# Kernel tuning notes

Hardware: AMD Instinct MI355X
Metric: run time of the kernel (lower is better)

The kernel has to match this reference:

```python
import jax, jax.numpy as jnp
import numpy as np

MODEL_DIM = 512
HEAD_NUM = 8
HEAD_DIM = 64
INNER_DIM = HEAD_NUM * HEAD_DIM  # 512
B, L, S = 4, 2048, 2048


def setup_inputs() -> dict:
    key = jax.random.key(0)
    ks = jax.random.split(key, 7)
    query = jax.random.normal(ks[0], (B, L, MODEL_DIM), dtype=jnp.float32)
    key_t = jax.random.normal(ks[1], (B, S, MODEL_DIM), dtype=jnp.float32)
    value = jax.random.normal(ks[2], (B, S, MODEL_DIM), dtype=jnp.float32)
    # nn.Linear weights stored as [out, in]; applied as x @ W.T
    sc = 1.0 / np.sqrt(MODEL_DIM)
    Wq = jax.random.uniform(ks[3], (INNER_DIM, MODEL_DIM), jnp.float32, -sc, sc)
    Wk = jax.random.uniform(ks[4], (INNER_DIM, MODEL_DIM), jnp.float32, -sc, sc)
    Wv = jax.random.uniform(ks[5], (INNER_DIM, MODEL_DIM), jnp.float32, -sc, sc)
    Wo = jax.random.uniform(ks[6], (MODEL_DIM, INNER_DIM), jnp.float32, -sc, sc)
    return {"query": query, "key": key_t, "value": value,
            "Wq": Wq, "Wk": Wk, "Wv": Wv, "Wo": Wo}


def reference(query, key, value, Wq, Wk, Wv, Wo):
    temperature = HEAD_DIM ** 0.5
    # projections: [b, n, inner]
    q = query @ Wq.T
    k = key @ Wk.T
    v = value @ Wv.T
    # split heads: b n (h d) -> b n h d
    q = q.reshape(B, L, HEAD_NUM, HEAD_DIM)
    k = k.reshape(B, S, HEAD_NUM, HEAD_DIM)
    v = v.reshape(B, S, HEAD_NUM, HEAD_DIM)
    # full attention (FullAttention): scores [b, l, s, h]
    qk = jnp.einsum('blhd,bshd->blsh', q / temperature, k)
    z = jax.nn.softmax(qk, axis=2)
    attended = jnp.einsum('blsh,bshd->blhd', z, v)
    # merge heads: b l h d -> b l (h d), then output projection
    attended = attended.reshape(B, L, INNER_DIM)
    return attended @ Wo.T
```

## Files before the change

kernel.cpp:

```cpp
#include <hip/hip_runtime.h>
#include <stdint.h>
#include <stddef.h>

#define NB 4
#define NL 2048
#define MODEL 512
#define NH 8
#define HD 64

#define QSCALE 0.18033688011112042f

typedef __attribute__((ext_vector_type(8))) short short8;
typedef __attribute__((ext_vector_type(8))) __bf16 bf16x8;
typedef __attribute__((ext_vector_type(4))) float f32x4;
typedef __attribute__((ext_vector_type(16))) float f32x16;
typedef __attribute__((ext_vector_type(2))) unsigned int u32x2;

static __device__ __forceinline__ unsigned short f2bf(float x) {
  union { float f; unsigned u; } v; v.f = x;
  unsigned r = v.u + 0x7FFFu + ((v.u >> 16) & 1u);
  return (unsigned short)(r >> 16);
}

static __device__ __forceinline__ unsigned cvtpk(float lo, float hi) {
  unsigned r;
  asm("v_cvt_pk_bf16_f32 %0, %1, %2" : "=v"(r) : "v"(lo), "v"(hi));
  return r;
}

static __device__ __forceinline__ f32x4 mfma16(short8 a, short8 b, f32x4 c) {
  return __builtin_amdgcn_mfma_f32_16x16x32_bf16(
      __builtin_bit_cast(bf16x8, a), __builtin_bit_cast(bf16x8, b), c, 0, 0, 0);
}

static __device__ __forceinline__ f32x16 mfma32(short8 a, short8 b, f32x16 c) {
  return __builtin_amdgcn_mfma_f32_32x32x16_bf16(
      __builtin_bit_cast(bf16x8, a), __builtin_bit_cast(bf16x8, b), c, 0, 0, 0);
}

#define GLOAD_LDS(gp, lp)                                                      \
  __builtin_amdgcn_global_load_lds(                                            \
      (const __attribute__((address_space(1))) void*)(gp),                     \
      (__attribute__((address_space(3))) void*)(lp), 16, 0, 0)

__global__ __launch_bounds__(256) void qkv512(const float* __restrict__ Aq,
                                              const float* __restrict__ Ak,
                                              const float* __restrict__ Av,
                                              const float* __restrict__ Wqp,
                                              const float* __restrict__ Wkp,
                                              const float* __restrict__ Wvp,
                                              unsigned short* __restrict__ Qo,
                                              unsigned short* __restrict__ Ko,
                                              unsigned short* __restrict__ Vto) {
  __shared__ unsigned short Alds[128][72];
  __shared__ unsigned short Wlds[128][72];

  const int which = blockIdx.x >> 8;
  const int bid = blockIdx.x & 255;
  const float* A = which == 0 ? Aq : which == 1 ? Ak : Av;
  const float* W = which == 0 ? Wqp : which == 1 ? Wkp : Wvp;

  const int tid = threadIdx.x;
  const int bn = bid & 3;
  const int bm = bid >> 2;
  const int mbase = bm * 128, nbase = bn * 128;
  const int wid = tid >> 6, lane = tid & 63;
  const int lo = lane & 15, grp = lane >> 4;
  const int wm = wid >> 1, wn = wid & 1;

  f32x4 acc[4][4] = {};

#pragma unroll 1
  for (int kb = 0; kb < 8; ++kb) {
#pragma unroll
    for (int it = 0; it < 8; ++it) {
      int id = tid + it * 256;
      int row = id >> 4, cg = id & 15;
      float4 v = *(const float4*)(A + (size_t)(mbase + row) * 512 + kb * 64 + cg * 4);
      uint2 w; w.x = cvtpk(v.x, v.y); w.y = cvtpk(v.z, v.w);
      *(uint2*)&Alds[row][cg * 4] = w;
    }
#pragma unroll
    for (int it = 0; it < 8; ++it) {
      int id = tid + it * 256;
      int row = id >> 4, cg = id & 15;
      float4 v = *(const float4*)(W + (size_t)(nbase + row) * 512 + kb * 64 + cg * 4);
      uint2 w; w.x = cvtpk(v.x, v.y); w.y = cvtpk(v.z, v.w);
      *(uint2*)&Wlds[row][cg * 4] = w;
    }
    __syncthreads();

#pragma unroll
    for (int kk = 0; kk < 2; ++kk) {
      short8 aw[4], ba[4];
#pragma unroll
      for (int f = 0; f < 4; ++f)
        aw[f] = *(const short8*)&Wlds[wn * 64 + f * 16 + lo][kk * 32 + grp * 8];
#pragma unroll
      for (int f = 0; f < 4; ++f)
        ba[f] = *(const short8*)&Alds[wm * 64 + f * 16 + lo][kk * 32 + grp * 8];
#pragma unroll
      for (int mf = 0; mf < 4; ++mf)
#pragma unroll
        for (int nf = 0; nf < 4; ++nf)
          acc[mf][nf] = mfma16(aw[nf], ba[mf], acc[mf][nf]);
    }
    __syncthreads();
  }

  const float scale = (which == 0) ? QSCALE : 1.0f;
#pragma unroll
  for (int mf = 0; mf < 4; ++mf)
#pragma unroll
    for (int nf = 0; nf < 4; ++nf) {
      int m = mbase + wm * 64 + mf * 16 + lo;
      int n0 = nbase + wn * 64 + nf * 16 + grp * 4;
      f32x4 a = acc[mf][nf];
      if (which < 2) {
        unsigned short* C = which == 0 ? Qo : Ko;
        uint2 w;
        w.x = cvtpk(a[0] * scale, a[1] * scale);
        w.y = cvtpk(a[2] * scale, a[3] * scale);
        *(uint2*)(C + (size_t)m * 512 + n0) = w;
      } else {
        int b = m >> 11, s = m & 2047;
#pragma unroll
        for (int i = 0; i < 4; ++i)
          Vto[((size_t)b * 512 + n0 + i) * 2048 + s] = f2bf(a[i]);
      }
    }
}

__global__ __launch_bounds__(256) void gemmWo(const unsigned short* __restrict__ A,
                                              const float* __restrict__ W,
                                              float* __restrict__ C) {
  __shared__ unsigned short Alds[128][72];
  __shared__ unsigned short Wlds[128][72];

  const int tid = threadIdx.x;
  const int bn = blockIdx.x & 3;
  const int bm = blockIdx.x >> 2;
  const int mbase = bm * 128, nbase = bn * 128;
  const int wid = tid >> 6, lane = tid & 63;
  const int lo = lane & 15, grp = lane >> 4;
  const int wm = wid >> 1, wn = wid & 1;

  f32x4 acc[4][4] = {};

#pragma unroll 1
  for (int kb = 0; kb < 8; ++kb) {
#pragma unroll
    for (int it = 0; it < 4; ++it) {
      int id = tid + it * 256;
      int row = id >> 3, cg = id & 7;
      uint4 v = *(const uint4*)(A + (size_t)(mbase + row) * 512 + kb * 64 + cg * 8);
      *(uint4*)&Alds[row][cg * 8] = v;
    }
#pragma unroll
    for (int it = 0; it < 8; ++it) {
      int id = tid + it * 256;
      int row = id >> 4, cg = id & 15;
      float4 v = *(const float4*)(W + (size_t)(nbase + row) * 512 + kb * 64 + cg * 4);
      uint2 w; w.x = cvtpk(v.x, v.y); w.y = cvtpk(v.z, v.w);
      *(uint2*)&Wlds[row][cg * 4] = w;
    }
    __syncthreads();

#pragma unroll
    for (int kk = 0; kk < 2; ++kk) {
      short8 aw[4], ba[4];
#pragma unroll
      for (int f = 0; f < 4; ++f)
        aw[f] = *(const short8*)&Wlds[wn * 64 + f * 16 + lo][kk * 32 + grp * 8];
#pragma unroll
      for (int f = 0; f < 4; ++f)
        ba[f] = *(const short8*)&Alds[wm * 64 + f * 16 + lo][kk * 32 + grp * 8];
#pragma unroll
      for (int mf = 0; mf < 4; ++mf)
#pragma unroll
        for (int nf = 0; nf < 4; ++nf)
          acc[mf][nf] = mfma16(aw[nf], ba[mf], acc[mf][nf]);
    }
    __syncthreads();
  }

#pragma unroll
  for (int mf = 0; mf < 4; ++mf)
#pragma unroll
    for (int nf = 0; nf < 4; ++nf) {
      int m = mbase + wm * 64 + mf * 16 + lo;
      int n0 = nbase + wn * 64 + nf * 16 + grp * 4;
      f32x4 a = acc[mf][nf];
      float4 o;
      o.x = a[0]; o.y = a[1]; o.z = a[2]; o.w = a[3];
      *(float4*)(C + (size_t)m * 512 + n0) = o;
    }
}

__global__ __launch_bounds__(256, 2) void attn64(const unsigned short* __restrict__ Qg,
                                                 const unsigned short* __restrict__ Kg,
                                                 const unsigned short* __restrict__ Vt,
                                                 unsigned short* __restrict__ Og) {
  __shared__ __align__(16) char LDS[65536];
  char* Kbase = LDS;
  char* Vbase = LDS + 32768;
  float* cb = (float*)LDS;

  const int tid = threadIdx.x;
  const int wid = tid >> 6, lane = tid & 63;
  const int ln31 = lane & 31, hl = lane >> 5;
  const int qh = wid & 1, sh = wid >> 1;

  const int lb = ((blockIdx.x & 7) << 6) | (blockIdx.x >> 3);
  const int bh = lb >> 4, qb = lb & 15;
  const int b = bh >> 3, h = bh & 7;

  const unsigned short* Kbh = Kg + (size_t)b * 2048 * 512 + h * 64;
  const unsigned short* Vbh = Vt + ((size_t)b * 512 + h * 64) * 2048;

  const int q0 = qb * 128 + qh * 64 + ln31;

  short8 qfA[4], qfB[4];
#pragma unroll
  for (int ks = 0; ks < 4; ++ks) {
    qfA[ks] = *(const short8*)(Qg + ((size_t)b * 2048 + q0) * 512 + h * 64 + ks * 16 + hl * 8);
    qfB[ks] = *(const short8*)(Qg + ((size_t)b * 2048 + q0 + 32) * 512 + h * 64 + ks * 16 + hl * 8);
  }

  const int srow = lane >> 3;
  const int schunk = (lane & 7) ^ srow;
  const unsigned short* kgp = Kbh + (size_t)(sh * 16 * 64 + qh * 32 + srow) * 512 + schunk * 8;
  const unsigned short* vgp = Vbh + (size_t)(qh * 32 + srow) * 2048 + sh * 16 * 64 + schunk * 8;
  char* kd = Kbase + sh * 16384;
  char* vd = Vbase + sh * 16384;
  const int wofs = qh * 4096;

  const int rb0 = ln31 * 128, rb1 = rb0 + 4096;
  const int sw = (ln31 & 7) << 4;
  const int hl16 = hl * 16;

  const short8 ones = {0x3F80, 0x3F80, 0x3F80, 0x3F80, 0x3F80, 0x3F80, 0x3F80, 0x3F80};
  f32x16 oA0 = {}, oA1 = {}, oB0 = {}, oB1 = {}, lA = {}, lB = {};

#pragma unroll
  for (int g = 0; g < 4; ++g) {
    GLOAD_LDS(kgp + (size_t)g * 8 * 512, kd + wofs + g * 1024);
    GLOAD_LDS(vgp + (size_t)g * 8 * 2048, vd + wofs + g * 1024);
  }
  __syncthreads();

  int cur = 0;
#pragma unroll 1
  for (int t = 0; t < 16; ++t) {
    if (t < 15) {
      const unsigned short* kp = kgp + (size_t)(t + 1) * 64 * 512;
      const unsigned short* vp = vgp + (t + 1) * 64;
      char* kdn = kd + (cur ^ 1) * 8192 + wofs;
      char* vdn = vd + (cur ^ 1) * 8192 + wofs;
#pragma unroll
      for (int g = 0; g < 4; ++g) {
        GLOAD_LDS(kp + (size_t)g * 8 * 512, kdn + g * 1024);
        GLOAD_LDS(vp + (size_t)g * 8 * 2048, vdn + g * 1024);
      }
    }

    const char* kr = kd + cur * 8192;
    const char* vr = vd + cur * 8192;

    f32x16 sA0 = {}, sA1 = {}, sB0 = {}, sB1 = {};
    __builtin_amdgcn_s_setprio(1);
#pragma unroll
    for (int ks = 0; ks < 4; ++ks) {
      short8 k0 = *(const short8*)(kr + rb0 + ((ks * 32 + hl16) ^ sw));
      short8 k1 = *(const short8*)(kr + rb1 + ((ks * 32 + hl16) ^ sw));
      sA0 = mfma32(k0, qfA[ks], sA0);
      sA1 = mfma32(k1, qfA[ks], sA1);
      sB0 = mfma32(k0, qfB[ks], sB0);
      sB1 = mfma32(k1, qfB[ks], sB1);
    }
    __builtin_amdgcn_s_setprio(0);

    unsigned cA0[8], cA1[8], cB0[8], cB1[8];
#pragma unroll
    for (int i = 0; i < 8; ++i)
      cA0[i] = cvtpk(__builtin_exp2f(sA0[2 * i]), __builtin_exp2f(sA0[2 * i + 1]));
#pragma unroll
    for (int i = 0; i < 8; ++i)
      cA1[i] = cvtpk(__builtin_exp2f(sA1[2 * i]), __builtin_exp2f(sA1[2 * i + 1]));
#pragma unroll
    for (int i = 0; i < 8; ++i)
      cB0[i] = cvtpk(__builtin_exp2f(sB0[2 * i]), __builtin_exp2f(sB0[2 * i + 1]));
#pragma unroll
    for (int i = 0; i < 8; ++i)
      cB1[i] = cvtpk(__builtin_exp2f(sB1[2 * i]), __builtin_exp2f(sB1[2 * i + 1]));

    {
      u32x2 r;
      r = __builtin_amdgcn_permlane32_swap(cA0[0], cA0[2], false, false); cA0[0] = r[0]; cA0[2] = r[1];
      r = __builtin_amdgcn_permlane32_swap(cA0[1], cA0[3], false, false); cA0[1] = r[0]; cA0[3] = r[1];
      r = __builtin_amdgcn_permlane32_swap(cA0[4], cA0[6], false, false); cA0[4] = r[0]; cA0[6] = r[1];
      r = __builtin_amdgcn_permlane32_swap(cA0[5], cA0[7], false, false); cA0[5] = r[0]; cA0[7] = r[1];
      r = __builtin_amdgcn_permlane32_swap(cA1[0], cA1[2], false, false); cA1[0] = r[0]; cA1[2] = r[1];
      r = __builtin_amdgcn_permlane32_swap(cA1[1], cA1[3], false, false); cA1[1] = r[0]; cA1[3] = r[1];
      r = __builtin_amdgcn_permlane32_swap(cA1[4], cA1[6], false, false); cA1[4] = r[0]; cA1[6] = r[1];
      r = __builtin_amdgcn_permlane32_swap(cA1[5], cA1[7], false, false); cA1[5] = r[0]; cA1[7] = r[1];
      r = __builtin_amdgcn_permlane32_swap(cB0[0], cB0[2], false, false); cB0[0] = r[0]; cB0[2] = r[1];
      r = __builtin_amdgcn_permlane32_swap(cB0[1], cB0[3], false, false); cB0[1] = r[0]; cB0[3] = r[1];
      r = __builtin_amdgcn_permlane32_swap(cB0[4], cB0[6], false, false); cB0[4] = r[0]; cB0[6] = r[1];
      r = __builtin_amdgcn_permlane32_swap(cB0[5], cB0[7], false, false); cB0[5] = r[0]; cB0[7] = r[1];
      r = __builtin_amdgcn_permlane32_swap(cB1[0], cB1[2], false, false); cB1[0] = r[0]; cB1[2] = r[1];
      r = __builtin_amdgcn_permlane32_swap(cB1[1], cB1[3], false, false); cB1[1] = r[0]; cB1[3] = r[1];
      r = __builtin_amdgcn_permlane32_swap(cB1[4], cB1[6], false, false); cB1[4] = r[0]; cB1[6] = r[1];
      r = __builtin_amdgcn_permlane32_swap(cB1[5], cB1[7], false, false); cB1[5] = r[0]; cB1[7] = r[1];
    }
    short8 pfA[4], pfB[4];
    {
      union { unsigned u[4]; short8 s; } t2;
      t2.u[0] = cA0[0]; t2.u[1] = cA0[1]; t2.u[2] = cA0[2]; t2.u[3] = cA0[3]; pfA[0] = t2.s;
      t2.u[0] = cA0[4]; t2.u[1] = cA0[5]; t2.u[2] = cA0[6]; t2.u[3] = cA0[7]; pfA[1] = t2.s;
      t2.u[0] = cA1[0]; t2.u[1] = cA1[1]; t2.u[2] = cA1[2]; t2.u[3] = cA1[3]; pfA[2] = t2.s;
      t2.u[0] = cA1[4]; t2.u[1] = cA1[5]; t2.u[2] = cA1[6]; t2.u[3] = cA1[7]; pfA[3] = t2.s;
      t2.u[0] = cB0[0]; t2.u[1] = cB0[1]; t2.u[2] = cB0[2]; t2.u[3] = cB0[3]; pfB[0] = t2.s;
      t2.u[0] = cB0[4]; t2.u[1] = cB0[5]; t2.u[2] = cB0[6]; t2.u[3] = cB0[7]; pfB[1] = t2.s;
      t2.u[0] = cB1[0]; t2.u[1] = cB1[1]; t2.u[2] = cB1[2]; t2.u[3] = cB1[3]; pfB[2] = t2.s;
      t2.u[0] = cB1[4]; t2.u[1] = cB1[5]; t2.u[2] = cB1[6]; t2.u[3] = cB1[7]; pfB[3] = t2.s;
    }

    __builtin_amdgcn_s_setprio(1);
#pragma unroll
    for (int ks = 0; ks < 4; ++ks) {
      short8 v0 = *(const short8*)(vr + rb0 + ((ks * 32 + hl16) ^ sw));
      short8 v1 = *(const short8*)(vr + rb1 + ((ks * 32 + hl16) ^ sw));
      oA0 = mfma32(v0, pfA[ks], oA0);
      oA1 = mfma32(v1, pfA[ks], oA1);
      oB0 = mfma32(v0, pfB[ks], oB0);
      oB1 = mfma32(v1, pfB[ks], oB1);
      lA = mfma32(ones, pfA[ks], lA);
      lB = mfma32(ones, pfB[ks], lB);
    }
    __builtin_amdgcn_s_setprio(0);

    __syncthreads();
    cur ^= 1;
  }

  float* myc = cb + (size_t)(qh * 64 + lane) * 68;
  if (sh == 1) {
    float4* c4 = (float4*)myc;
#pragma unroll
    for (int i = 0; i < 4; ++i) {
      c4[i]      = make_float4(oA0[4*i], oA0[4*i+1], oA0[4*i+2], oA0[4*i+3]);
      c4[4 + i]  = make_float4(oA1[4*i], oA1[4*i+1], oA1[4*i+2], oA1[4*i+3]);
      c4[8 + i]  = make_float4(oB0[4*i], oB0[4*i+1], oB0[4*i+2], oB0[4*i+3]);
      c4[12 + i] = make_float4(oB1[4*i], oB1[4*i+1], oB1[4*i+2], oB1[4*i+3]);
    }
    myc[64] = lA[0]; myc[65] = lB[0];
  }
  __syncthreads();
  if (sh == 0) {
#pragma unroll
    for (int i = 0; i < 16; ++i) {
      oA0[i] += myc[i];      oA1[i] += myc[16 + i];
      oB0[i] += myc[32 + i]; oB1[i] += myc[48 + i];
    }
    float invA = 1.f / (lA[0] + myc[64]);
    float invB = 1.f / (lB[0] + myc[65]);

#pragma unroll
    for (int dblk = 0; dblk < 2; ++dblk) {
      const f32x16& a = dblk ? oA1 : oA0;
      const f32x16& bb = dblk ? oB1 : oB0;
#pragma unroll
      for (int rg = 0; rg < 4; ++rg) {
        int d0 = dblk * 32 + rg * 8 + hl * 4;
        uint2 w;
        w.x = cvtpk(a[rg * 4 + 0] * invA, a[rg * 4 + 1] * invA);
        w.y = cvtpk(a[rg * 4 + 2] * invA, a[rg * 4 + 3] * invA);
        *(uint2*)(Og + ((size_t)b * 2048 + q0) * 512 + h * 64 + d0) = w;
        w.x = cvtpk(bb[rg * 4 + 0] * invB, bb[rg * 4 + 1] * invB);
        w.y = cvtpk(bb[rg * 4 + 2] * invB, bb[rg * 4 + 3] * invB);
        *(uint2*)(Og + ((size_t)b * 2048 + q0 + 32) * 512 + h * 64 + d0) = w;
      }
    }
  }
}

extern "C" void kernel_launch(void* const* d_in, const int* in_sizes, int n_in,
                              void* d_out, int out_size, void* d_ws, size_t ws_size,
                              hipStream_t stream) {
  (void)in_sizes; (void)n_in; (void)out_size; (void)ws_size;
  const float* query = (const float*)d_in[0];
  const float* key   = (const float*)d_in[1];
  const float* value = (const float*)d_in[2];
  const float* Wq    = (const float*)d_in[3];
  const float* Wk    = (const float*)d_in[4];
  const float* Wv    = (const float*)d_in[5];
  const float* Wo    = (const float*)d_in[6];

  const size_t TOK = (size_t)NB * NL * MODEL;
  unsigned short* Qw = (unsigned short*)d_ws;
  unsigned short* Kw = Qw + TOK;
  unsigned short* Vw = Kw + TOK;
  unsigned short* Aw = Vw + TOK;

  qkv512<<<768, 256, 0, stream>>>(query, key, value, Wq, Wk, Wv, Qw, Kw, Vw);
  attn64<<<512, 256, 0, stream>>>(Qw, Kw, Vw, Aw);
  gemmWo<<<256, 256, 0, stream>>>(Aw, Wo, (float*)d_out);
}
```

Measured before the change: 118.0 us.

## Split attention tile into halves to interleave softmax with PV MFMAs; widen gemmWo blocks

The attention inner loop now computes QK scores and exp/permlane packing in two 32-key halves, so the PV MFMAs for the first half can be issued while the second half's exponentials are still being computed. The s_setprio hints are removed. The aim is more overlap between VALU transcendental work and matrix-core work, and lower peak register pressure. Separately, the output-projection GEMM moves from 256 to 512 threads per block, each wave holding a 64x32 tile instead of 64x64, which adds waves for latency hiding but reuses less data per wave.

```diff
diff --git a/kernel.cpp b/kernel.cpp
--- a/kernel.cpp
+++ b/kernel.cpp
@@ -131,7 +131,7 @@
     }
 }
 
-__global__ __launch_bounds__(256) void gemmWo(const unsigned short* __restrict__ A,
+__global__ __launch_bounds__(512) void gemmWo(const unsigned short* __restrict__ A,
                                               const float* __restrict__ W,
                                               float* __restrict__ C) {
   __shared__ unsigned short Alds[128][72];
@@ -143,22 +143,22 @@
   const int mbase = bm * 128, nbase = bn * 128;
   const int wid = tid >> 6, lane = tid & 63;
   const int lo = lane & 15, grp = lane >> 4;
-  const int wm = wid >> 1, wn = wid & 1;
-
-  f32x4 acc[4][4] = {};
+  const int wm = wid >> 2, wn = wid & 3;
+
+  f32x4 acc[4][2] = {};
 
 #pragma unroll 1
   for (int kb = 0; kb < 8; ++kb) {
 #pragma unroll
-    for (int it = 0; it < 4; ++it) {
-      int id = tid + it * 256;
+    for (int it = 0; it < 2; ++it) {
+      int id = tid + it * 512;
       int row = id >> 3, cg = id & 7;
       uint4 v = *(const uint4*)(A + (size_t)(mbase + row) * 512 + kb * 64 + cg * 8);
       *(uint4*)&Alds[row][cg * 8] = v;
     }
 #pragma unroll
-    for (int it = 0; it < 8; ++it) {
-      int id = tid + it * 256;
+    for (int it = 0; it < 4; ++it) {
+      int id = tid + it * 512;
       int row = id >> 4, cg = id & 15;
       float4 v = *(const float4*)(W + (size_t)(nbase + row) * 512 + kb * 64 + cg * 4);
       uint2 w; w.x = cvtpk(v.x, v.y); w.y = cvtpk(v.z, v.w);
@@ -168,17 +168,17 @@
 
 #pragma unroll
     for (int kk = 0; kk < 2; ++kk) {
-      short8 aw[4], ba[4];
-#pragma unroll
-      for (int f = 0; f < 4; ++f)
-        aw[f] = *(const short8*)&Wlds[wn * 64 + f * 16 + lo][kk * 32 + grp * 8];
+      short8 aw[2], ba[4];
+#pragma unroll
+      for (int f = 0; f < 2; ++f)
+        aw[f] = *(const short8*)&Wlds[wn * 32 + f * 16 + lo][kk * 32 + grp * 8];
 #pragma unroll
       for (int f = 0; f < 4; ++f)
         ba[f] = *(const short8*)&Alds[wm * 64 + f * 16 + lo][kk * 32 + grp * 8];
 #pragma unroll
       for (int mf = 0; mf < 4; ++mf)
 #pragma unroll
-        for (int nf = 0; nf < 4; ++nf)
+        for (int nf = 0; nf < 2; ++nf)
           acc[mf][nf] = mfma16(aw[nf], ba[mf], acc[mf][nf]);
     }
     __syncthreads();
@@ -187,9 +187,9 @@
 #pragma unroll
   for (int mf = 0; mf < 4; ++mf)
 #pragma unroll
-    for (int nf = 0; nf < 4; ++nf) {
+    for (int nf = 0; nf < 2; ++nf) {
       int m = mbase + wm * 64 + mf * 16 + lo;
-      int n0 = nbase + wn * 64 + nf * 16 + grp * 4;
+      int n0 = nbase + wn * 32 + nf * 16 + grp * 4;
       f32x4 a = acc[mf][nf];
       float4 o;
       o.x = a[0]; o.y = a[1]; o.z = a[2]; o.w = a[3];
@@ -267,78 +267,102 @@
     const char* kr = kd + cur * 8192;
     const char* vr = vd + cur * 8192;
 
-    f32x16 sA0 = {}, sA1 = {}, sB0 = {}, sB1 = {};
-    __builtin_amdgcn_s_setprio(1);
+    f32x16 sA0 = {}, sB0 = {};
 #pragma unroll
     for (int ks = 0; ks < 4; ++ks) {
       short8 k0 = *(const short8*)(kr + rb0 + ((ks * 32 + hl16) ^ sw));
+      sA0 = mfma32(k0, qfA[ks], sA0);
+      sB0 = mfma32(k0, qfB[ks], sB0);
+    }
+    f32x16 sA1 = {}, sB1 = {};
+#pragma unroll
+    for (int ks = 0; ks < 4; ++ks) {
       short8 k1 = *(const short8*)(kr + rb1 + ((ks * 32 + hl16) ^ sw));
-      sA0 = mfma32(k0, qfA[ks], sA0);
       sA1 = mfma32(k1, qfA[ks], sA1);
-      sB0 = mfma32(k0, qfB[ks], sB0);
       sB1 = mfma32(k1, qfB[ks], sB1);
     }
-    __builtin_amdgcn_s_setprio(0);
-
-    unsigned cA0[8], cA1[8], cB0[8], cB1[8];
+
+    unsigned cA0[8], cB0[8];
 #pragma unroll
     for (int i = 0; i < 8; ++i)
       cA0[i] = cvtpk(__builtin_exp2f(sA0[2 * i]), __builtin_exp2f(sA0[2 * i + 1]));
 #pragma unroll
     for (int i = 0; i < 8; ++i)
-      cA1[i] = cvtpk(__builtin_exp2f(sA1[2 * i]), __builtin_exp2f(sA1[2 * i + 1]));
-#pragma unroll
-    for (int i = 0; i < 8; ++i)
       cB0[i] = cvtpk(__builtin_exp2f(sB0[2 * i]), __builtin_exp2f(sB0[2 * i + 1]));
-#pragma unroll
-    for (int i = 0; i < 8; ++i)
-      cB1[i] = cvtpk(__builtin_exp2f(sB1[2 * i]), __builtin_exp2f(sB1[2 * i + 1]));
-
     {
       u32x2 r;
       r = __builtin_amdgcn_permlane32_swap(cA0[0], cA0[2], false, false); cA0[0] = r[0]; cA0[2] = r[1];
       r = __builtin_amdgcn_permlane32_swap(cA0[1], cA0[3], false, false); cA0[1] = r[0]; cA0[3] = r[1];
       r = __builtin_amdgcn_permlane32_swap(cA0[4], cA0[6], false, false); cA0[4] = r[0]; cA0[6] = r[1];
       r = __builtin_amdgcn_permlane32_swap(cA0[5], cA0[7], false, false); cA0[5] = r[0]; cA0[7] = r[1];
+      r = __builtin_amdgcn_permlane32_swap(cB0[0], cB0[2], false, false); cB0[0] = r[0]; cB0[2] = r[1];
+      r = __builtin_amdgcn_permlane32_swap(cB0[1], cB0[3], false, false); cB0[1] = r[0]; cB0[3] = r[1];
+      r = __builtin_amdgcn_permlane32_swap(cB0[4], cB0[6], false, false); cB0[4] = r[0]; cB0[6] = r[1];
+      r = __builtin_amdgcn_permlane32_swap(cB0[5], cB0[7], false, false); cB0[5] = r[0]; cB0[7] = r[1];
+    }
+    short8 pfA0, pfA1, pfB0, pfB1;
+    {
+      union { unsigned u[4]; short8 s; } t2;
+      t2.u[0] = cA0[0]; t2.u[1] = cA0[1]; t2.u[2] = cA0[2]; t2.u[3] = cA0[3]; pfA0 = t2.s;
+      t2.u[0] = cA0[4]; t2.u[1] = cA0[5]; t2.u[2] = cA0[6]; t2.u[3] = cA0[7]; pfA1 = t2.s;
+      t2.u[0] = cB0[0]; t2.u[1] = cB0[1]; t2.u[2] = cB0[2]; t2.u[3] = cB0[3]; pfB0 = t2.s;
+      t2.u[0] = cB0[4]; t2.u[1] = cB0[5]; t2.u[2] = cB0[6]; t2.u[3] = cB0[7]; pfB1 = t2.s;
+    }
+
+#pragma unroll
+    for (int ks = 0; ks < 2; ++ks) {
+      short8 pf = ks ? pfA1 : pfA0;
+      short8 pg = ks ? pfB1 : pfB0;
+      short8 v0 = *(const short8*)(vr + rb0 + ((ks * 32 + hl16) ^ sw));
+      short8 v1 = *(const short8*)(vr + rb1 + ((ks * 32 + hl16) ^ sw));
+      oA0 = mfma32(v0, pf, oA0);
+      oA1 = mfma32(v1, pf, oA1);
+      oB0 = mfma32(v0, pg, oB0);
+      oB1 = mfma32(v1, pg, oB1);
+      lA = mfma32(ones, pf, lA);
+      lB = mfma32(ones, pg, lB);
+    }
+
+    unsigned cA1[8], cB1[8];
+#pragma unroll
+    for (int i = 0; i < 8; ++i)
+      cA1[i] = cvtpk(__builtin_exp2f(sA1[2 * i]), __builtin_exp2f(sA1[2 * i + 1]));
+#pragma unroll
+    for (int i = 0; i < 8; ++i)
+      cB1[i] = cvtpk(__builtin_exp2f(sB1[2 * i]), __builtin_exp2f(sB1[2 * i + 1]));
+    {
+      u32x2 r;
       r = __builtin_amdgcn_permlane32_swap(cA1[0], cA1[2], false, false); cA1[0] = r[0]; cA1[2] = r[1];
       r = __builtin_amdgcn_permlane32_swap(cA1[1], cA1[3], false, false); cA1[1] = r[0]; cA1[3] = r[1];
       r = __builtin_amdgcn_permlane32_swap(cA1[4], cA1[6], false, false); cA1[4] = r[0]; cA1[6] = r[1];
       r = __builtin_amdgcn_permlane32_swap(cA1[5], cA1[7], false, false); cA1[5] = r[0]; cA1[7] = r[1];
-      r = __builtin_amdgcn_permlane32_swap(cB0[0], cB0[2], false, false); cB0[0] = r[0]; cB0[2] = r[1];
-      r = __builtin_amdgcn_permlane32_swap(cB0[1], cB0[3], false, false); cB0[1] = r[0]; cB0[3] = r[1];
-      r = __builtin_amdgcn_permlane32_swap(cB0[4], cB0[6], false, false); cB0[4] = r[0]; cB0[6] = r[1];
-      r = __builtin_amdgcn_permlane32_swap(cB0[5], cB0[7], false, false); cB0[5] = r[0]; cB0[7] = r[1];
       r = __builtin_amdgcn_permlane32_swap(cB1[0], cB1[2], false, false); cB1[0] = r[0]; cB1[2] = r[1];
       r = __builtin_amdgcn_permlane32_swap(cB1[1], cB1[3], false, false); cB1[1] = r[0]; cB1[3] = r[1];
       r = __builtin_amdgcn_permlane32_swap(cB1[4], cB1[6], false, false); cB1[4] = r[0]; cB1[6] = r[1];
       r = __builtin_amdgcn_permlane32_swap(cB1[5], cB1[7], false, false); cB1[5] = r[0]; cB1[7] = r[1];
     }
-    short8 pfA[4], pfB[4];
+    short8 pfA2, pfA3, pfB2, pfB3;
     {
       union { unsigned u[4]; short8 s; } t2;
-      t2.u[0] = cA0[0]; t2.u[1] = cA0[1]; t2.u[2] = cA0[2]; t2.u[3] = cA0[3]; pfA[0] = t2.s;
-      t2.u[0] = cA0[4]; t2.u[1] = cA0[5]; t2.u[2] = cA0[6]; t2.u[3] = cA0[7]; pfA[1] = t2.s;
-      t2.u[0] = cA1[0]; t2.u[1] = cA1[1]; t2.u[2] = cA1[2]; t2.u[3] = cA1[3]; pfA[2] = t2.s;
-      t2.u[0] = cA1[4]; t2.u[1] = cA1[5]; t2.u[2] = cA1[6]; t2.u[3] = cA1[7]; pfA[3] = t2.s;
-      t2.u[0] = cB0[0]; t2.u[1] = cB0[1]; t2.u[2] = cB0[2]; t2.u[3] = cB0[3]; pfB[0] = t2.s;
-      t2.u[0] = cB0[4]; t2.u[1] = cB0[5]; t2.u[2] = cB0[6]; t2.u[3] = cB0[7]; pfB[1] = t2.s;
-      t2.u[0] = cB1[0]; t2.u[1] = cB1[1]; t2.u[2] = cB1[2]; t2.u[3] = cB1[3]; pfB[2] = t2.s;
-      t2.u[0] = cB1[4]; t2.u[1] = cB1[5]; t2.u[2] = cB1[6]; t2.u[3] = cB1[7]; pfB[3] = t2.s;
-    }
-
-    __builtin_amdgcn_s_setprio(1);
-#pragma unroll
-    for (int ks = 0; ks < 4; ++ks) {
+      t2.u[0] = cA1[0]; t2.u[1] = cA1[1]; t2.u[2] = cA1[2]; t2.u[3] = cA1[3]; pfA2 = t2.s;
+      t2.u[0] = cA1[4]; t2.u[1] = cA1[5]; t2.u[2] = cA1[6]; t2.u[3] = cA1[7]; pfA3 = t2.s;
+      t2.u[0] = cB1[0]; t2.u[1] = cB1[1]; t2.u[2] = cB1[2]; t2.u[3] = cB1[3]; pfB2 = t2.s;
+      t2.u[0] = cB1[4]; t2.u[1] = cB1[5]; t2.u[2] = cB1[6]; t2.u[3] = cB1[7]; pfB3 = t2.s;
+    }
+
+#pragma unroll
+    for (int ks = 2; ks < 4; ++ks) {
+      short8 pf = (ks == 2) ? pfA2 : pfA3;
+      short8 pg = (ks == 2) ? pfB2 : pfB3;
       short8 v0 = *(const short8*)(vr + rb0 + ((ks * 32 + hl16) ^ sw));
       short8 v1 = *(const short8*)(vr + rb1 + ((ks * 32 + hl16) ^ sw));
-      oA0 = mfma32(v0, pfA[ks], oA0);
-      oA1 = mfma32(v1, pfA[ks], oA1);
-      oB0 = mfma32(v0, pfB[ks], oB0);
-      oB1 = mfma32(v1, pfB[ks], oB1);
-      lA = mfma32(ones, pfA[ks], lA);
-      lB = mfma32(ones, pfB[ks], lB);
-    }
-    __builtin_amdgcn_s_setprio(0);
+      oA0 = mfma32(v0, pf, oA0);
+      oA1 = mfma32(v1, pf, oA1);
+      oB0 = mfma32(v0, pg, oB0);
+      oB1 = mfma32(v1, pg, oB1);
+      lA = mfma32(ones, pf, lA);
+      lB = mfma32(ones, pg, lB);
+    }
 
     __syncthreads();
     cur ^= 1;
@@ -405,5 +429,5 @@
 
   qkv512<<<768, 256, 0, stream>>>(query, key, value, Wq, Wk, Wv, Qw, Kw, Vw);
   attn64<<<512, 256, 0, stream>>>(Qw, Kw, Vw, Aw);
-  gemmWo<<<256, 256, 0, stream>>>(Aw, Wo, (float*)d_out);
-}
+  gemmWo<<<256, 512, 0, stream>>>(Aw, Wo, (float*)d_out);
+}
```

Result: faster. 115.1 us (-2.5%).
